# Kernel tuning notes

Measured on AMD Instinct MI355X. Metric: run time of the kernel, lower is better.

## Reference

```python
import jax, jax.numpy as jnp
import numpy as np

B, N, D = 2, 8192, 32
RADIUS2 = 0.03 ** 2
SIM_THRESH = 0.7
MIN_LEAF = 10
EPS = 1e-8


def setup_inputs() -> dict:
    key = jax.random.key(0)
    ks = jax.random.split(key, 5)
    # points scaled to [0, 0.4)^3 so the 0.03 radius finds a few neighbors per point
    points = jax.random.uniform(ks[0], (B, N, 3), dtype=jnp.float32) * 0.4
    embeddings = jax.random.normal(ks[1], (B, N, D), dtype=jnp.float32)
    leaf_mask = jax.random.randint(ks[2], (B, N), 0, 2).astype(jnp.int32)
    # consistency_net: Linear(2D -> D), ReLU, Linear(D -> D); stored as (in, out)
    W1 = jax.random.normal(ks[3], (2 * D, D), dtype=jnp.float32) / np.sqrt(2 * D)
    b1 = jnp.zeros((D,), dtype=jnp.float32)
    W2 = jax.random.normal(ks[4], (D, D), dtype=jnp.float32) / np.sqrt(D)
    b2 = jnp.zeros((D,), dtype=jnp.float32)
    return {"points": points, "embeddings": embeddings, "leaf_mask": leaf_mask,
            "W1": W1, "b1": b1, "W2": W2, "b2": b2}


def reference(points, embeddings, leaf_mask, W1, b1, W2, b2):
    leaf = leaf_mask > 0  # [B,N]
    # squared pairwise distances via ||a||^2 + ||b||^2 - 2 a.b (avoids [B,N,N,3])
    sq = jnp.sum(points * points, axis=-1)  # [B,N]
    d2 = sq[:, :, None] + sq[:, None, :] - 2.0 * jnp.einsum('bnc,bmc->bnm', points, points)
    nb = (d2 < RADIUS2) & leaf[:, None, :]  # neighbor j must be a leaf point
    nb_count = jnp.sum(nb, axis=-1)  # includes self when leaf[i]
    # cosine similarity with per-vector norm clamp (torch F.cosine_similarity eps)
    norms = jnp.maximum(jnp.linalg.norm(embeddings, axis=-1, keepdims=True), EPS)
    en = embeddings / norms
    sim = jnp.einsum('bnd,bmd->bnm', en, en)
    similar = nb & (sim > SIM_THRESH)
    cnt = jnp.sum(similar, axis=-1)  # [B,N]
    w = similar.astype(embeddings.dtype)
    mean_sim = jnp.einsum('bnm,bmd->bnd', w, embeddings) / jnp.maximum(cnt, 1)[..., None]
    combined = jnp.concatenate([embeddings, mean_sim], axis=-1)  # [B,N,2D]
    h = jax.nn.relu(combined @ W1 + b1)
    out = h @ W2 + b2
    batch_ok = (jnp.sum(leaf, axis=-1) >= MIN_LEAF)[:, None]  # skip batches with <10 leaves
    cond = leaf & (nb_count > 1) & (cnt > 0) & batch_ok
    return jnp.where(cond[..., None], out, embeddings)
```

## Files before the change

kernel.cpp:

```cpp
#include <hip/hip_runtime.h>

#define NPTS 8192
#define BN   16384
#define D    32
#define R2   0.0009f
#define SIMT 0.7f
#define RAD  0.03f
#define BLOCK 256
#define PBLOCK 1024
#define PWAVES 16
#define ZBINS 512
#define ZSCALE 1280.0f
#define AFIELDS 34

__global__ __launch_bounds__(BLOCK) void histscan_kernel(
    const float* __restrict__ pts, const float* __restrict__ emb,
    const int* __restrict__ leaf, float* __restrict__ invn,
    int* __restrict__ histA, int* __restrict__ histL,
    int* __restrict__ leafcnt, unsigned* __restrict__ done,
    int* __restrict__ rsA, int* __restrict__ rsL,
    int* __restrict__ curA, int* __restrict__ curL) {
  const int p = blockIdx.x * BLOCK + threadIdx.x;
  const float z = pts[3 * p + 2];
  int bin = (int)(z * ZSCALE); if (bin > ZBINS - 1) bin = ZBINS - 1;
  const int b = p >> 13;
  const int lf = leaf[p] > 0;
  atomicAdd(&histA[b * ZBINS + bin], 1);
  if (lf) atomicAdd(&histL[b * ZBINS + bin], 1);

  const float4* er = (const float4*)(emb + (size_t)p * D);
  float ss = 0.f;
#pragma unroll
  for (int i = 0; i < D / 4; ++i) {
    float4 v = er[i];
    ss += v.x * v.x + v.y * v.y + v.z * v.z + v.w * v.w;
  }
  invn[p] = 1.0f / fmaxf(sqrtf(ss), 1e-8f);

  const unsigned long long m = __ballot(lf);
  if ((threadIdx.x & 63) == 0) atomicAdd(&leafcnt[b], (int)__popcll(m));

  __shared__ int islast;
  __threadfence();
  if (threadIdx.x == 0) {
    const unsigned t = __hip_atomic_fetch_add(done, 1u, __ATOMIC_ACQ_REL,
                                              __HIP_MEMORY_SCOPE_AGENT);
    islast = (t == gridDim.x - 1);
  }
  __syncthreads();
  if (!islast) return;

  const int wv = threadIdx.x >> 6;
  const int lane = threadIdx.x & 63;
  const int sb = wv & 1;
  const int* __restrict__ h = (wv < 2) ? histA : histL;
  int* __restrict__ rs = (wv < 2) ? rsA : rsL;
  int* __restrict__ cu = (wv < 2) ? curA : curL;
  int carry = 0;
  for (int c = 0; c < ZBINS / 64; ++c) {
    const int idx = c * 64 + lane;
    const int v = __hip_atomic_load(&h[sb * ZBINS + idx], __ATOMIC_RELAXED,
                                    __HIP_MEMORY_SCOPE_AGENT);
    int incl = v;
#pragma unroll
    for (int off = 1; off < 64; off <<= 1) {
      const int t = __shfl_up(incl, off);
      if (lane >= off) incl += t;
    }
    const int excl = carry + incl - v;
    rs[sb * (ZBINS + 1) + idx] = excl;
    cu[sb * ZBINS + idx] = excl;
    carry += __shfl(incl, 63);
  }
  if (lane == 0) rs[sb * (ZBINS + 1) + ZBINS] = carry;
}

__global__ __launch_bounds__(BLOCK) void scatter_kernel(
    const float* __restrict__ pts, const float* __restrict__ emb,
    const int* __restrict__ leaf, const float* __restrict__ invn,
    int* __restrict__ curA, int* __restrict__ curL,
    float4* __restrict__ sortedA, int* __restrict__ permA,
    float4* __restrict__ pts4L, float* __restrict__ invL,
    float* __restrict__ embL) {
  const int p = blockIdx.x * BLOCK + threadIdx.x;
  const float x = pts[3 * p + 0];
  const float y = pts[3 * p + 1];
  const float z = pts[3 * p + 2];
  const float sq = x * x + y * y + z * z;
  const int lf = leaf[p] > 0;
  const float inv = invn[p];
  int bin = (int)(z * ZSCALE); if (bin > ZBINS - 1) bin = ZBINS - 1;
  const int b = p >> 13;

  const int dst = b * NPTS + atomicAdd(&curA[b * ZBINS + bin], 1);
  sortedA[dst] = make_float4(x, y, z, lf ? inv : -inv);
  permA[dst] = p;

  if (lf) {
    const int dl = b * NPTS + atomicAdd(&curL[b * ZBINS + bin], 1);
    pts4L[dl] = make_float4(x, y, z, 0.5f * (sq - R2));
    invL[dl] = inv;
    const float4* __restrict__ s4 = (const float4*)(emb + (size_t)p * D);
    float4* __restrict__ d4 = (float4*)(embL + (size_t)dl * D);
#pragma unroll
    for (int k = 0; k < D / 4; ++k) d4[k] = s4[k];
  }
}

__global__ __launch_bounds__(PBLOCK) void pair_kernel(
    const float4* __restrict__ sortedA, const int* __restrict__ permA,
    const float4* __restrict__ pts4L, const float* __restrict__ invL,
    const float* __restrict__ embL, const float* __restrict__ emb,
    const int* __restrict__ rsL, const int* __restrict__ leafcnt,
    const float* __restrict__ W1, const float* __restrict__ b1,
    const float* __restrict__ W2, const float* __restrict__ b2,
    float* __restrict__ out) {
  const int ig   = blockIdx.x;
  const int b    = ig >> 7;
  const int lane = threadIdx.x & 63;
  const int wv   = threadIdx.x >> 6;
  const int sg   = ig * 64 + lane;

  __shared__ float red[AFIELDS][64];
  for (int t = threadIdx.x; t < AFIELDS * 64; t += PBLOCK)
    (&red[0][0])[t] = 0.f;
  __syncthreads();

  const float4 A = sortedA[sg];
  const float inv_i = fabsf(A.w);
  const float mhsq = -0.5f * (A.x * A.x + A.y * A.y + A.z * A.z);
  const int p = permA[sg];

  float4 ei[D / 4];
  {
    const float4* __restrict__ e4 = (const float4*)(emb + (size_t)p * D);
#pragma unroll
    for (int k = 0; k < D / 4; ++k) ei[k] = e4[k];
  }

  float zmin = A.z, zmax = A.z;
#pragma unroll
  for (int off = 1; off < 64; off <<= 1) {
    zmin = fminf(zmin, __shfl_xor(zmin, off));
    zmax = fmaxf(zmax, __shfl_xor(zmax, off));
  }
  int klo = (int)((zmin - RAD) * ZSCALE) - 1; if (klo < 0) klo = 0;
  int khi = (int)((zmax + RAD) * ZSCALE) + 1; if (khi > ZBINS - 1) khi = ZBINS - 1;
  klo = __builtin_amdgcn_readfirstlane(klo);
  khi = __builtin_amdgcn_readfirstlane(khi);
  const int jlo = b * NPTS + rsL[b * (ZBINS + 1) + klo];
  const int jhi = b * NPTS + rsL[b * (ZBINS + 1) + khi + 1];
  const int len = jhi - jlo;
  int c0 = jlo + (len * wv) / PWAVES;
  int c1 = jlo + (len * (wv + 1)) / PWAVES;
  c0 = __builtin_amdgcn_readfirstlane(c0);
  c1 = __builtin_amdgcn_readfirstlane(c1);

  float acc[D];
#pragma unroll
  for (int d = 0; d < D; ++d) acc[d] = 0.f;
  float nbc = 0.f, cnt = 0.f;

  auto process = [&](const float4 c, const int jj) {
    const float t = fmaf(A.z, c.z, fmaf(A.y, c.y, fmaf(A.x, c.x, mhsq)));
    if (t > c.w) {
      nbc += 1.0f;
      const float4* __restrict__ ej4 = (const float4*)(embL + (size_t)jj * D);
      float s0 = 0.f, s1 = 0.f, s2 = 0.f, s3 = 0.f;
#pragma unroll
      for (int k = 0; k < D / 4; ++k) {
        const float4 vj = ej4[k];
        s0 = fmaf(ei[k].x, vj.x, s0);
        s1 = fmaf(ei[k].y, vj.y, s1);
        s2 = fmaf(ei[k].z, vj.z, s2);
        s3 = fmaf(ei[k].w, vj.w, s3);
      }
      const float s = ((s0 + s1) + (s2 + s3)) * inv_i * invL[jj];
      if (s > SIMT) {
        cnt += 1.0f;
#pragma unroll
        for (int k = 0; k < D / 4; ++k) {
          const float4 vj = ej4[k];
          acc[4 * k + 0] += vj.x;
          acc[4 * k + 1] += vj.y;
          acc[4 * k + 2] += vj.z;
          acc[4 * k + 3] += vj.w;
        }
      }
    }
  };

  const int nfull = (c1 - c0) & ~7;
  if (nfull > 0) {
    float4 cur[8], nxt[8];
#pragma unroll
    for (int u = 0; u < 8; ++u) cur[u] = pts4L[c0 + u];
    for (int j = c0; j < c0 + nfull; j += 8) {
      const int jn = (j + 8 < c0 + nfull) ? (j + 8) : c0;
#pragma unroll
      for (int u = 0; u < 8; ++u) nxt[u] = pts4L[jn + u];
#pragma unroll
      for (int u = 0; u < 8; ++u) process(cur[u], j + u);
#pragma unroll
      for (int u = 0; u < 8; ++u) cur[u] = nxt[u];
    }
  }
  for (int j = c0 + nfull; j < c1; ++j) process(pts4L[j], j);

  if (nbc != 0.f) atomicAdd(&red[0][lane], nbc);
  if (cnt != 0.f) {
    atomicAdd(&red[1][lane], cnt);
#pragma unroll
    for (int d = 0; d < D; ++d) atomicAdd(&red[2 + d][lane], acc[d]);
  }
  __syncthreads();

  if (threadIdx.x < 64) {
    const float tnbc = red[0][lane];
    const float tcnt = red[1][lane];
    const float rinv = 1.0f / fmaxf(tcnt, 1.0f);

    float e[D];
#pragma unroll
    for (int k = 0; k < D / 4; ++k) {
      e[4 * k + 0] = ei[k].x; e[4 * k + 1] = ei[k].y;
      e[4 * k + 2] = ei[k].z; e[4 * k + 3] = ei[k].w;
    }

    float h[D];
#pragma unroll
    for (int k = 0; k < D; ++k) h[k] = b1[k];
    for (int d = 0; d < D; ++d) {
      const float c = e[d];
      const float* __restrict__ w = W1 + (size_t)d * D;
#pragma unroll
      for (int k = 0; k < D; ++k) h[k] = fmaf(c, w[k], h[k]);
    }
    for (int d = 0; d < D; ++d) {
      const float c = red[2 + d][lane] * rinv;
      const float* __restrict__ w = W1 + (size_t)(D + d) * D;
#pragma unroll
      for (int k = 0; k < D; ++k) h[k] = fmaf(c, w[k], h[k]);
    }
#pragma unroll
    for (int k = 0; k < D; ++k) h[k] = fmaxf(h[k], 0.f);

    float o[D];
#pragma unroll
    for (int m = 0; m < D; ++m) o[m] = b2[m];
    for (int k = 0; k < D; ++k) {
      const float c = h[k];
      const float* __restrict__ w = W2 + (size_t)k * D;
#pragma unroll
      for (int m = 0; m < D; ++m) o[m] = fmaf(c, w[m], o[m]);
    }

    const bool lf = A.w > 0.f;
    const bool cond = lf && (tnbc >= 2.0f) && (tcnt >= 1.0f) && (leafcnt[b] >= 10);

    float4* outr = (float4*)(out + (size_t)p * D);
#pragma unroll
    for (int i = 0; i < D / 4; ++i) {
      float4 v;
      if (cond) { v.x = o[4*i+0]; v.y = o[4*i+1]; v.z = o[4*i+2]; v.w = o[4*i+3]; }
      else      { v = ei[i]; }
      outr[i] = v;
    }
  }
}

extern "C" void kernel_launch(void* const* d_in, const int* in_sizes, int n_in,
                              void* d_out, int out_size, void* d_ws, size_t ws_size,
                              hipStream_t stream) {
  (void)in_sizes; (void)n_in; (void)out_size; (void)ws_size;
  const float* pts  = (const float*)d_in[0];
  const float* emb  = (const float*)d_in[1];
  const int*   leaf = (const int*)d_in[2];
  const float* W1   = (const float*)d_in[3];
  const float* b1   = (const float*)d_in[4];
  const float* W2   = (const float*)d_in[5];
  const float* b2   = (const float*)d_in[6];
  float* out = (float*)d_out;

  char* ws = (char*)d_ws;
  size_t off = 0;
  auto alloc = [&](size_t bytes) { void* r = ws + off; off = (off + bytes + 15) & ~(size_t)15; return r; };

  float4*   sortedA = (float4*)alloc((size_t)BN * 16);
  int*      permA   = (int*)alloc((size_t)BN * 4);
  float4*   pts4L   = (float4*)alloc((size_t)BN * 16);
  float*    invL    = (float*)alloc((size_t)BN * 4);
  float*    embL    = (float*)alloc((size_t)BN * D * 4);
  float*    invn    = (float*)alloc((size_t)BN * 4);
  int*      rsA     = (int*)alloc(2 * (ZBINS + 1) * 4);
  int*      rsL     = (int*)alloc(2 * (ZBINS + 1) * 4);
  int*      curA    = (int*)alloc(2 * ZBINS * 4);
  int*      curL    = (int*)alloc(2 * ZBINS * 4);
  int*      histA   = (int*)alloc(2 * ZBINS * 4);
  int*      histL   = (int*)alloc(2 * ZBINS * 4);
  int*      leafcnt = (int*)alloc(16);
  unsigned* done    = (unsigned*)alloc(16);

  hipMemsetAsync(histA, 0, 2 * (2 * ZBINS * 4) + 32, stream);
  histscan_kernel<<<BN / BLOCK, BLOCK, 0, stream>>>(
      pts, emb, leaf, invn, histA, histL, leafcnt, done, rsA, rsL, curA, curL);
  scatter_kernel<<<BN / BLOCK, BLOCK, 0, stream>>>(
      pts, emb, leaf, invn, curA, curL, sortedA, permA, pts4L, invL, embL);
  pair_kernel<<<BN / 64, PBLOCK, 0, stream>>>(
      sortedA, permA, pts4L, invL, embL, emb, rsL, leafcnt,
      W1, b1, W2, b2, out);
}
```

Measured before the change: 123.0 us.

## Stage candidate points and embeddings into LDS with double-buffered async loads

The pair kernel now copies chunks of 160 candidate leaf points (positions, inverse norms, embeddings) from global memory into double-buffered LDS using global_load_lds. All 16 waves share each staged chunk, and the next chunk is prefetched while the current one is processed. Before, each wave read its own slice straight from global/L2. The change adds a block barrier per chunk and about 45KB of LDS per block, which may lower occupancy. Workspace buffers are padded so the last chunk's over-read stays in bounds.

```diff
diff --git a/kernel.cpp b/kernel.cpp
--- a/kernel.cpp
+++ b/kernel.cpp
@@ -9,9 +9,23 @@
 #define BLOCK 256
 #define PBLOCK 1024
 #define PWAVES 16
+#define NGRP   (BN / 64)
 #define ZBINS 512
 #define ZSCALE 1280.0f
 #define AFIELDS 34
+#define CHUNK 160
+
+#define GLOBAL_AS __attribute__((address_space(1)))
+#define LDS_AS    __attribute__((address_space(3)))
+
+__device__ __forceinline__ void g2lds16(const void* g, void* l) {
+  __builtin_amdgcn_global_load_lds((const GLOBAL_AS void*)g, (LDS_AS void*)l,
+                                   16, 0, 0);
+}
+__device__ __forceinline__ void g2lds4(const void* g, void* l) {
+  __builtin_amdgcn_global_load_lds((const GLOBAL_AS void*)g, (LDS_AS void*)l,
+                                   4, 0, 0);
+}
 
 __global__ __launch_bounds__(BLOCK) void histscan_kernel(
     const float* __restrict__ pts, const float* __restrict__ emb,
@@ -121,10 +135,12 @@
   const int wv   = threadIdx.x >> 6;
   const int sg   = ig * 64 + lane;
 
+  __shared__ __align__(16) float4 embS[2][CHUNK * 8];
+  __shared__ __align__(16) float4 ptsS[2][192];
+  __shared__ float invS[2][192];
   __shared__ float red[AFIELDS][64];
   for (int t = threadIdx.x; t < AFIELDS * 64; t += PBLOCK)
     (&red[0][0])[t] = 0.f;
-  __syncthreads();
 
   const float4 A = sortedA[sg];
   const float inv_i = fabsf(A.w);
@@ -151,61 +167,83 @@
   const int jlo = b * NPTS + rsL[b * (ZBINS + 1) + klo];
   const int jhi = b * NPTS + rsL[b * (ZBINS + 1) + khi + 1];
   const int len = jhi - jlo;
-  int c0 = jlo + (len * wv) / PWAVES;
-  int c1 = jlo + (len * (wv + 1)) / PWAVES;
-  c0 = __builtin_amdgcn_readfirstlane(c0);
-  c1 = __builtin_amdgcn_readfirstlane(c1);
 
   float acc[D];
 #pragma unroll
   for (int d = 0; d < D; ++d) acc[d] = 0.f;
   float nbc = 0.f, cnt = 0.f;
 
-  auto process = [&](const float4 c, const int jj) {
-    const float t = fmaf(A.z, c.z, fmaf(A.y, c.y, fmaf(A.x, c.x, mhsq)));
-    if (t > c.w) {
-      nbc += 1.0f;
-      const float4* __restrict__ ej4 = (const float4*)(embL + (size_t)jj * D);
-      float s0 = 0.f, s1 = 0.f, s2 = 0.f, s3 = 0.f;
-#pragma unroll
-      for (int k = 0; k < D / 4; ++k) {
-        const float4 vj = ej4[k];
-        s0 = fmaf(ei[k].x, vj.x, s0);
-        s1 = fmaf(ei[k].y, vj.y, s1);
-        s2 = fmaf(ei[k].z, vj.z, s2);
-        s3 = fmaf(ei[k].w, vj.w, s3);
-      }
-      const float s = ((s0 + s1) + (s2 + s3)) * inv_i * invL[jj];
-      if (s > SIMT) {
-        cnt += 1.0f;
+  auto stage = [&](int buf, int base, int L) {
+    const int nf4 = L * 8;
+    for (int t0 = wv * 64; t0 < nf4; t0 += PWAVES * 64)
+      g2lds16((const char*)embL + (((size_t)base * 8 + t0 + lane) << 4),
+              &embS[buf][t0]);
+    for (int t0 = wv * 64; t0 < L; t0 += PWAVES * 64)
+      g2lds16((const char*)pts4L + (((size_t)base + t0 + lane) << 4),
+              &ptsS[buf][t0]);
+    {
+      const int t0 = (wv - 4) * 64;
+      if (t0 >= 0 && t0 < L)
+        g2lds4((const char*)invL + (((size_t)base + t0 + lane) << 2),
+               &invS[buf][t0]);
+    }
+  };
+
+  auto process = [&](int buf, int L) {
+    const int s0 = (L * wv) / PWAVES;
+    const int s1 = (L * (wv + 1)) / PWAVES;
+    if (s0 >= s1) return;
+    float4 c = ptsS[buf][s0];
+    for (int jl = s0; jl < s1; ++jl) {
+      const float4 cn = ptsS[buf][(jl + 1 < s1) ? (jl + 1) : s0];
+      const float t = fmaf(A.z, c.z, fmaf(A.y, c.y, fmaf(A.x, c.x, mhsq)));
+      if (t > c.w) {
+        nbc += 1.0f;
+        const float4* __restrict__ ej4 = &embS[buf][jl * 8];
+        float s0_ = 0.f, s1_ = 0.f, s2_ = 0.f, s3_ = 0.f;
 #pragma unroll
         for (int k = 0; k < D / 4; ++k) {
           const float4 vj = ej4[k];
-          acc[4 * k + 0] += vj.x;
-          acc[4 * k + 1] += vj.y;
-          acc[4 * k + 2] += vj.z;
-          acc[4 * k + 3] += vj.w;
+          s0_ = fmaf(ei[k].x, vj.x, s0_);
+          s1_ = fmaf(ei[k].y, vj.y, s1_);
+          s2_ = fmaf(ei[k].z, vj.z, s2_);
+          s3_ = fmaf(ei[k].w, vj.w, s3_);
+        }
+        const float sm = ((s0_ + s1_) + (s2_ + s3_)) * inv_i * invS[buf][jl];
+        if (sm > SIMT) {
+          cnt += 1.0f;
+#pragma unroll
+          for (int k = 0; k < D / 4; ++k) {
+            const float4 vj = ej4[k];
+            acc[4 * k + 0] += vj.x;
+            acc[4 * k + 1] += vj.y;
+            acc[4 * k + 2] += vj.z;
+            acc[4 * k + 3] += vj.w;
+          }
         }
       }
+      c = cn;
     }
   };
 
-  const int nfull = (c1 - c0) & ~7;
-  if (nfull > 0) {
-    float4 cur[8], nxt[8];
-#pragma unroll
-    for (int u = 0; u < 8; ++u) cur[u] = pts4L[c0 + u];
-    for (int j = c0; j < c0 + nfull; j += 8) {
-      const int jn = (j + 8 < c0 + nfull) ? (j + 8) : c0;
-#pragma unroll
-      for (int u = 0; u < 8; ++u) nxt[u] = pts4L[jn + u];
-#pragma unroll
-      for (int u = 0; u < 8; ++u) process(cur[u], j + u);
-#pragma unroll
-      for (int u = 0; u < 8; ++u) cur[u] = nxt[u];
-    }
-  }
-  for (int j = c0 + nfull; j < c1; ++j) process(pts4L[j], j);
+  const int nch = (len + CHUNK - 1) / CHUNK;
+  if (nch > 0) {
+    stage(0, jlo, (len < CHUNK) ? len : CHUNK);
+    __syncthreads();
+    for (int k = 0; k < nch; ++k) {
+      const int cur = k & 1;
+      if (k + 1 < nch) {
+        const int base = jlo + (k + 1) * CHUNK;
+        const int L = (jhi - base < CHUNK) ? (jhi - base) : CHUNK;
+        stage(cur ^ 1, base, L);
+      }
+      const int Lc = (len - k * CHUNK < CHUNK) ? (len - k * CHUNK) : CHUNK;
+      process(cur, Lc);
+      __syncthreads();
+    }
+  } else {
+    __syncthreads();
+  }
 
   if (nbc != 0.f) atomicAdd(&red[0][lane], nbc);
   if (cnt != 0.f) {
@@ -288,9 +326,9 @@
 
   float4*   sortedA = (float4*)alloc((size_t)BN * 16);
   int*      permA   = (int*)alloc((size_t)BN * 4);
-  float4*   pts4L   = (float4*)alloc((size_t)BN * 16);
-  float*    invL    = (float*)alloc((size_t)BN * 4);
-  float*    embL    = (float*)alloc((size_t)BN * D * 4);
+  float4*   pts4L   = (float4*)alloc((size_t)(BN + CHUNK) * 16);
+  float*    invL    = (float*)alloc((size_t)(BN + CHUNK) * 4);
+  float*    embL    = (float*)alloc((size_t)(BN + CHUNK) * D * 4);
   float*    invn    = (float*)alloc((size_t)BN * 4);
   int*      rsA     = (int*)alloc(2 * (ZBINS + 1) * 4);
   int*      rsL     = (int*)alloc(2 * (ZBINS + 1) * 4);
@@ -306,7 +344,7 @@
       pts, emb, leaf, invn, histA, histL, leafcnt, done, rsA, rsL, curA, curL);
   scatter_kernel<<<BN / BLOCK, BLOCK, 0, stream>>>(
       pts, emb, leaf, invn, curA, curL, sortedA, permA, pts4L, invL, embL);
-  pair_kernel<<<BN / 64, PBLOCK, 0, stream>>>(
+  pair_kernel<<<NGRP, PBLOCK, 0, stream>>>(
       sortedA, permA, pts4L, invL, embL, emb, rsL, leafcnt,
       W1, b1, W2, b2, out);
 }
```

Result: slower. 134.2 us (+9.1%).
